# Optimization experiments

Hardware: AMD Instinct MI355X
Metric: run time of the kernel (lower is better)

## Reference

```python
import jax, jax.numpy as jnp
import numpy as np
import math

N, T, D, H = 64, 512, 1024, 1024

def setup_inputs() -> dict:
    key = jax.random.key(0)
    k1, k2, k3, k4 = jax.random.split(key, 4)
    x = jax.random.normal(k1, (N, T, D), dtype=jnp.float32)
    h0 = jax.random.normal(k2, (N, H), dtype=jnp.float32)
    Wx = jax.random.normal(k3, (D, 4 * H), dtype=jnp.float32) / math.sqrt(D)
    Wh = jax.random.normal(k4, (H, 4 * H), dtype=jnp.float32) / math.sqrt(H)
    b = jnp.zeros((4 * H,), dtype=jnp.float32)
    return {"x": x, "h0": h0, "Wx": Wx, "Wh": Wh, "b": b}

def lstm_forward(x, h0, Wx, Wh, b):
    Hd = h0.shape[1]
    # Precompute input-to-hidden contribution for all timesteps in one GEMM.
    xW = jnp.einsum('ntd,dg->ntg', x, Wx) + b  # (N, T, 4H)
    c0 = jnp.zeros_like(h0)

    def step(carry, xw_t):
        prev_h, prev_c = carry
        a = xw_t + prev_h @ Wh  # (N, 4H)
        i = jax.nn.sigmoid(a[:, :Hd])
        f = jax.nn.sigmoid(a[:, Hd:2 * Hd])
        o = jax.nn.sigmoid(a[:, 2 * Hd:3 * Hd])
        g = jnp.tanh(a[:, 3 * Hd:])
        next_c = f * prev_c + i * g
        next_h = o * jnp.tanh(next_c)
        return (next_h, next_c), next_h

    # scan over time axis: move T to leading dim
    (_, _), hs = jax.lax.scan(step, (h0, c0), jnp.swapaxes(xW, 0, 1))
    return jnp.swapaxes(hs, 0, 1)  # (N, T, H)

def reference(x, h0, Wx, Wh, b):
    return lstm_forward(x, h0, Wx, Wh, b)
```

## Files before the change

kernel.cpp:

```cpp
#include <hip/hip_runtime.h>


#define NB 64
#define TT 512
#define DD 1024
#define HH 1024
#define GG 4096
#define FSTRIDE 32
#define NCHUNK 256
#define CSTRIDE 8

using f32x4  = __attribute__((ext_vector_type(4))) float;
using bf16x8 = __attribute__((ext_vector_type(8))) __bf16;
using u16x4  = __attribute__((ext_vector_type(4))) unsigned short;

__device__ inline unsigned short f2bf(float x) {
  union { float f; unsigned u; } v; v.f = x;
  unsigned r = v.u + 0x7fffu + ((v.u >> 16) & 1u);
  return (unsigned short)(r >> 16);
}
__device__ inline float bfu2f(unsigned short u) {
  union { unsigned u; float f; } v; v.u = ((unsigned)u) << 16; return v.f;
}
__device__ inline float sigm(float x)     { return 1.0f / (1.0f + __expf(-x)); }
__device__ inline float tanhfast(float x) { return 1.0f - 2.0f / (__expf(2.0f * x) + 1.0f); }

__global__ __launch_bounds__(256) void tcast(const float* __restrict__ in,
                                             unsigned short* __restrict__ out,
                                             int rows, int cols) {
  __shared__ float tile[32][33];
  const int bx = blockIdx.x * 32;
  const int by = blockIdx.y * 32;
  const int tx = threadIdx.x;
  for (int i = threadIdx.y; i < 32; i += 8)
    tile[i][tx] = in[(size_t)(by + i) * cols + bx + tx];
  __syncthreads();
  for (int i = threadIdx.y; i < 32; i += 8)
    out[(size_t)(bx + i) * rows + by + tx] = f2bf(tile[tx][i]);
}

__global__ __launch_bounds__(256) void init_h(const float* __restrict__ h0,
                                              unsigned* __restrict__ hp0,
                                              unsigned* __restrict__ hp1,
                                              int* __restrict__ bar) {
  const int idx = blockIdx.x * 256 + threadIdx.x;
  const float v = h0[idx];
  const unsigned short hi = f2bf(v);
  const unsigned short lo = f2bf(v - bfu2f(hi));
  hp0[idx] = ((unsigned)hi << 16) | ((unsigned)(lo & 0xFFFEu));
  hp1[idx] = 1u;
  if (blockIdx.x == 0)
    for (int i = threadIdx.x; i < 256 * FSTRIDE + NCHUNK * CSTRIDE; i += 256)
      bar[i] = 0;
}

__global__ __launch_bounds__(512, 1) void lstm_fused(
    const float* __restrict__ x,
    const unsigned short* __restrict__ WxT,
    const unsigned short* __restrict__ WhT,
    const float* __restrict__ bvec,
    unsigned short* __restrict__ xw,
    unsigned* __restrict__ hp0, unsigned* __restrict__ hp1,
    float* __restrict__ out, int* __restrict__ bar) {
  __shared__ __align__(16) unsigned char smem[74240];
  const int tid = threadIdx.x;
  const int bid = blockIdx.x;
  int* cnt = bar + 256 * FSTRIDE;

  if (bid >= 128) {
    unsigned short (*As)[72] = (unsigned short(*)[72])smem;
    unsigned short (*Bs)[72] = (unsigned short(*)[72])(smem + 18432);
    const int gid  = bid - 128;
    const int wave = tid >> 6, lane = tid & 63;
    const int wm = (wave & 1) * 64, wn = (wave >> 1) * 32;
    const int lr = lane & 15, lk = (lane >> 4) * 8;

    for (int tau = gid; tau < NCHUNK * 32; tau += 128) {
      const int c  = tau >> 5;
      const int n  = tau & 31;
      const int m0 = c * 128;
      const int g0 = n * 128;
      f32x4 acc[4][2] = {};

      for (int kt = 0; kt < DD; kt += 64) {
#pragma unroll
        for (int it = 0; it < 4; ++it) {
          const int rl = it * 32 + (tid >> 4);
          const int c4 = (tid & 15) * 4;
          const int m  = m0 + rl;
          const size_t xrow = (size_t)(m & 63) * TT + (m >> 6);
          const float4 xv = *(const float4*)(x + xrow * DD + kt + c4);
          u16x4 us; us.x = f2bf(xv.x); us.y = f2bf(xv.y);
          us.z = f2bf(xv.z); us.w = f2bf(xv.w);
          *(u16x4*)&As[rl][c4] = us;
        }
#pragma unroll
        for (int it = 0; it < 2; ++it) {
          const int rl = it * 64 + (tid >> 3);
          const int c8 = (tid & 7) * 8;
          const uint4 wv = *(const uint4*)(WxT + (size_t)(g0 + rl) * DD + kt + c8);
          *(uint4*)&Bs[rl][c8] = wv;
        }
        __syncthreads();
#pragma unroll
        for (int ks = 0; ks < 2; ++ks) {
          const int kk = ks * 32 + lk;
          bf16x8 af[4], bfv[2];
#pragma unroll
          for (int mi = 0; mi < 4; ++mi) af[mi]  = *(const bf16x8*)&As[wm + mi * 16 + lr][kk];
#pragma unroll
          for (int ni = 0; ni < 2; ++ni) bfv[ni] = *(const bf16x8*)&Bs[wn + ni * 16 + lr][kk];
#pragma unroll
          for (int mi = 0; mi < 4; ++mi)
#pragma unroll
            for (int ni = 0; ni < 2; ++ni)
              acc[mi][ni] = __builtin_amdgcn_mfma_f32_16x16x32_bf16(af[mi], bfv[ni], acc[mi][ni], 0, 0, 0);
        }
        __syncthreads();
      }

#pragma unroll
      for (int mi = 0; mi < 4; ++mi) {
        const int row = m0 + wm + mi * 16 + ((lane >> 4) << 2);
#pragma unroll
        for (int ni = 0; ni < 2; ++ni) {
          const int col = g0 + wn + ni * 16 + lr;
          const float bb = bvec[col];
#pragma unroll
          for (int j = 0; j < 4; ++j)
            xw[(size_t)(row + j) * GG + col] = f2bf(acc[mi][ni][j] + bb);
        }
      }
      __syncthreads();
      if (tid == 0) {
        __builtin_amdgcn_fence(__ATOMIC_RELEASE, "agent");
        __hip_atomic_fetch_add(&cnt[c * CSTRIDE], 1,
                               __ATOMIC_RELAXED, __HIP_MEMORY_SCOPE_AGENT);
      }
    }
    return;
  }

  unsigned short (*As_hi)[1024] = (unsigned short(*)[1024])smem;
  unsigned short (*As_lo)[1024] = (unsigned short(*)[1024])(smem + 32768);
  float (*abuf)[16][34] = (float(*)[16][34])(smem + 65536);

  const int grp  = bid & 3;
  const int qid  = bid >> 2;
  const int r0   = grp * 16;
  const int j0   = qid * 32;
  const int w    = tid >> 6;
  const int gate = w & 3;
  const int ch   = w >> 2;
  const int lane = tid & 63;
  const int lr   = lane & 15;
  const int kslot = lane >> 4;
  const int sx   = lr & 7;
  const int srow = tid >> 5;
  const int swr  = srow & 7;
  const int re   = tid >> 5, ce = tid & 31;

  int* myflag = &bar[(grp * 32 + qid) * FSTRIDE];

  bf16x8 rB[32];
  {
    const unsigned short* wrow =
        WhT + ((size_t)(gate * HH + j0 + ch * 16 + lr)) * HH + kslot * 8;
#pragma unroll
    for (int ks = 0; ks < 32; ++ks)
      rB[ks] = *(const bf16x8*)&wrow[ks * 32];
  }

  float creg = 0.0f;

  const size_t xrowc = (size_t)(r0 + re) * GG + j0 + ce;
#define XWADDR(u, g) ((size_t)(u) * ((size_t)NB * GG) + xrowc + (size_t)(g) * HH)

  int last_c = 0;
  if (tid == 32) {
    while (__hip_atomic_load(&cnt[0], __ATOMIC_RELAXED, __HIP_MEMORY_SCOPE_AGENT) < 32)
      __builtin_amdgcn_s_sleep(2);
  }
  __syncthreads();
  unsigned short xc0 = xw[XWADDR(0, 0)];
  unsigned short xc1 = xw[XWADDR(0, 1)];
  unsigned short xc2 = xw[XWADDR(0, 2)];
  unsigned short xc3 = xw[XWADDR(0, 3)];

  for (int t = 0; t < TT; ++t) {
    unsigned* hp = (t & 1) ? hp1 : hp0;
    unsigned* np = (t & 1) ? hp0 : hp1;

    if (t > 0 && tid < 32) {
      const int* fp = &bar[(grp * 32 + tid) * FSTRIDE];
      int v = __hip_atomic_load(fp, __ATOMIC_RELAXED, __HIP_MEMORY_SCOPE_AGENT);
      while (v < t) {
        __builtin_amdgcn_s_sleep(2);
        v = __hip_atomic_load(fp, __ATOMIC_RELAXED, __HIP_MEMORY_SCOPE_AGENT);
      }
    }
    if (tid == 32) {
      const int u = (t + 1 < TT) ? (t + 1) : (TT - 1);
      const int cn = u >> 1;
      if (cn > last_c) {
        while (__hip_atomic_load(&cnt[cn * CSTRIDE],
                                 __ATOMIC_RELAXED, __HIP_MEMORY_SCOPE_AGENT) < 32)
          __builtin_amdgcn_s_sleep(2);
        last_c = cn;
      }
    }
    __syncthreads();

    const unsigned* hrow = hp + (size_t)(r0 + srow) * HH;
    const int c0 = 0 * 32 + (tid & 31), c1 = 1 * 32 + (tid & 31);
    const int c2 = 2 * 32 + (tid & 31), c3 = 3 * 32 + (tid & 31);
    const unsigned* p0 = hrow + c0 * 8;
    const unsigned* p1 = hrow + c1 * 8;
    const unsigned* p2 = hrow + c2 * 8;
    const unsigned* p3 = hrow + c3 * 8;
    const unsigned expect = (unsigned)((t >> 1) & 1);
    uint4 q0, q1, q2, q3, q4, q5, q6, q7;
    for (;;) {
      asm volatile(
          "global_load_dwordx4 %0, %[a0], off sc0 sc1\n\t"
          "global_load_dwordx4 %1, %[a0], off offset:16 sc0 sc1\n\t"
          "global_load_dwordx4 %2, %[a1], off sc0 sc1\n\t"
          "global_load_dwordx4 %3, %[a1], off offset:16 sc0 sc1\n\t"
          "global_load_dwordx4 %4, %[a2], off sc0 sc1\n\t"
          "global_load_dwordx4 %5, %[a2], off offset:16 sc0 sc1\n\t"
          "global_load_dwordx4 %6, %[a3], off sc0 sc1\n\t"
          "global_load_dwordx4 %7, %[a3], off offset:16 sc0 sc1\n\t"
          "s_waitcnt vmcnt(0)"
          : "=&v"(q0), "=&v"(q1), "=&v"(q2), "=&v"(q3),
            "=&v"(q4), "=&v"(q5), "=&v"(q6), "=&v"(q7)
          : [a0] "v"(p0), [a1] "v"(p1), [a2] "v"(p2), [a3] "v"(p3)
          : "memory");
      const unsigned av = q0.x & q0.y & q0.z & q0.w & q1.x & q1.y & q1.z & q1.w &
                          q2.x & q2.y & q2.z & q2.w & q3.x & q3.y & q3.z & q3.w &
                          q4.x & q4.y & q4.z & q4.w & q5.x & q5.y & q5.z & q5.w &
                          q6.x & q6.y & q6.z & q6.w & q7.x & q7.y & q7.z & q7.w;
      const unsigned ov = q0.x | q0.y | q0.z | q0.w | q1.x | q1.y | q1.z | q1.w |
                          q2.x | q2.y | q2.z | q2.w | q3.x | q3.y | q3.z | q3.w |
                          q4.x | q4.y | q4.z | q4.w | q5.x | q5.y | q5.z | q5.w |
                          q6.x | q6.y | q6.z | q6.w | q7.x | q7.y | q7.z | q7.w;
      const unsigned chk = expect ? av : ~ov;
      if (chk & 1u) break;
      __builtin_amdgcn_s_sleep(1);
    }

#define UNPACK(QA, QB, CC)                                                    \
    {                                                                         \
      const int sc = (CC) ^ swr;                                              \
      uint4 HI, LO;                                                           \
      HI.x = (QA.x >> 16) | (QA.y & 0xffff0000u);                             \
      HI.y = (QA.z >> 16) | (QA.w & 0xffff0000u);                             \
      HI.z = (QB.x >> 16) | (QB.y & 0xffff0000u);                             \
      HI.w = (QB.z >> 16) | (QB.w & 0xffff0000u);                             \
      LO.x = (QA.x & 0xffffu) | (QA.y << 16);                                 \
      LO.y = (QA.z & 0xffffu) | (QA.w << 16);                                 \
      LO.z = (QB.x & 0xffffu) | (QB.y << 16);                                 \
      LO.w = (QB.z & 0xffffu) | (QB.w << 16);                                 \
      *(uint4*)&As_hi[srow][sc * 8] = HI;                                     \
      *(uint4*)&As_lo[srow][sc * 8] = LO;                                     \
    }
    UNPACK(q0, q1, c0) UNPACK(q2, q3, c1) UNPACK(q4, q5, c2) UNPACK(q6, q7, c3)
#undef UNPACK
    __syncthreads();

    const int tn = (t + 1 < TT) ? t + 1 : t;
    const unsigned short nx0 = xw[XWADDR(tn, 0)];
    const unsigned short nx1 = xw[XWADDR(tn, 1)];
    const unsigned short nx2 = xw[XWADDR(tn, 2)];
    const unsigned short nx3 = xw[XWADDR(tn, 3)];

    f32x4 aHE = {}, aHO = {}, aLE = {}, aLO = {};
#pragma unroll
    for (int ks = 0; ks < 32; ks += 2) {
      const int cc0 = ((ks)     * 4 + kslot) ^ sx;
      const int cc1 = ((ks + 1) * 4 + kslot) ^ sx;
      const bf16x8 ah0 = *(const bf16x8*)&As_hi[lr][cc0 * 8];
      const bf16x8 al0 = *(const bf16x8*)&As_lo[lr][cc0 * 8];
      const bf16x8 ah1 = *(const bf16x8*)&As_hi[lr][cc1 * 8];
      const bf16x8 al1 = *(const bf16x8*)&As_lo[lr][cc1 * 8];
      aHE = __builtin_amdgcn_mfma_f32_16x16x32_bf16(ah0, rB[ks],     aHE, 0, 0, 0);
      aLE = __builtin_amdgcn_mfma_f32_16x16x32_bf16(al0, rB[ks],     aLE, 0, 0, 0);
      aHO = __builtin_amdgcn_mfma_f32_16x16x32_bf16(ah1, rB[ks + 1], aHO, 0, 0, 0);
      aLO = __builtin_amdgcn_mfma_f32_16x16x32_bf16(al1, rB[ks + 1], aLO, 0, 0, 0);
    }
    const f32x4 accv = (aHE + aHO) + (aLE + aLO);

#pragma unroll
    for (int j = 0; j < 4; ++j)
      abuf[gate][(lane >> 4) * 4 + j][ch * 16 + lr] = accv[j];
    __syncthreads();

    const float ai = abuf[0][re][ce] + bfu2f(xc0);
    const float af = abuf[1][re][ce] + bfu2f(xc1);
    const float ao = abuf[2][re][ce] + bfu2f(xc2);
    const float ag = abuf[3][re][ce] + bfu2f(xc3);

    const float gi = sigm(ai), gf = sigm(af), go = sigm(ao), gg = tanhfast(ag);
    creg = gf * creg + gi * gg;
    const float hn = go * tanhfast(creg);

    out[((size_t)(r0 + re) * TT + t) * HH + j0 + ce] = hn;
    const unsigned short hi = f2bf(hn);
    const unsigned short lo = f2bf(hn - bfu2f(hi));
    const unsigned tag = (unsigned)(((t + 1) >> 1) & 1);
    const unsigned pack = ((unsigned)hi << 16) | ((unsigned)(lo & 0xFFFEu) | tag);
    __hip_atomic_store(&np[(size_t)(r0 + re) * HH + j0 + ce], pack,
                       __ATOMIC_RELAXED, __HIP_MEMORY_SCOPE_AGENT);

    xc0 = nx0; xc1 = nx1; xc2 = nx2; xc3 = nx3;

    if (t + 1 < TT) {
      __syncthreads();
      if (tid == 0)
        __hip_atomic_store(myflag, t + 1, __ATOMIC_RELAXED, __HIP_MEMORY_SCOPE_AGENT);
    }
  }
#undef XWADDR
}

extern "C" void kernel_launch(void* const* d_in, const int* in_sizes, int n_in,
                              void* d_out, int out_size, void* d_ws, size_t ws_size,
                              hipStream_t stream) {
  const float* x  = (const float*)d_in[0];
  const float* h0 = (const float*)d_in[1];
  const float* Wx = (const float*)d_in[2];
  const float* Wh = (const float*)d_in[3];
  const float* b  = (const float*)d_in[4];
  float* out = (float*)d_out;

  const size_t xw_elems = (size_t)NB * TT * GG;
  const size_t wT_elems = (size_t)GG * DD;
  const size_t NH       = (size_t)NB * HH;

  unsigned short* xw  = (unsigned short*)d_ws;
  unsigned short* WxT = xw + xw_elems;
  unsigned short* WhT = WxT + wT_elems;
  unsigned* hp0 = (unsigned*)(WhT + wT_elems);
  unsigned* hp1 = hp0 + NH;
  int* bar = (int*)(hp1 + NH);

  tcast<<<dim3(GG / 32, DD / 32), dim3(32, 8), 0, stream>>>(Wx, WxT, DD, GG);
  tcast<<<dim3(GG / 32, HH / 32), dim3(32, 8), 0, stream>>>(Wh, WhT, HH, GG);
  init_h<<<NB * HH / 256, 256, 0, stream>>>(h0, hp0, hp1, bar);

  lstm_fused<<<256, 512, 0, stream>>>(x, WxT, WhT, b, xw, hp0, hp1, out, bar);
}
```

Before: 2.681 ms.

## Fuse weight transpose-cast into persistent LSTM kernel and busy-spin step flags

Removes the two separate transpose-and-cast kernel launches. The 128 GEMM blocks inside the fused kernel now transpose Wx and Wh to bf16 themselves and publish completion through a new device-wide counter. Recurrent blocks wait on that counter before loading Wh into registers. The per-step flag polling also drops s_sleep and spins tightly, aiming to cut wake-up latency per timestep at the cost of more memory traffic from polling.

```diff
diff --git a/kernel.cpp b/kernel.cpp
--- a/kernel.cpp
+++ b/kernel.cpp
@@ -24,20 +24,6 @@
 }
 __device__ inline float sigm(float x)     { return 1.0f / (1.0f + __expf(-x)); }
 __device__ inline float tanhfast(float x) { return 1.0f - 2.0f / (__expf(2.0f * x) + 1.0f); }
-
-__global__ __launch_bounds__(256) void tcast(const float* __restrict__ in,
-                                             unsigned short* __restrict__ out,
-                                             int rows, int cols) {
-  __shared__ float tile[32][33];
-  const int bx = blockIdx.x * 32;
-  const int by = blockIdx.y * 32;
-  const int tx = threadIdx.x;
-  for (int i = threadIdx.y; i < 32; i += 8)
-    tile[i][tx] = in[(size_t)(by + i) * cols + bx + tx];
-  __syncthreads();
-  for (int i = threadIdx.y; i < 32; i += 8)
-    out[(size_t)(bx + i) * rows + by + tx] = f2bf(tile[tx][i]);
-}
 
 __global__ __launch_bounds__(256) void init_h(const float* __restrict__ h0,
                                               unsigned* __restrict__ hp0,
@@ -50,27 +36,67 @@
   hp0[idx] = ((unsigned)hi << 16) | ((unsigned)(lo & 0xFFFEu));
   hp1[idx] = 1u;
   if (blockIdx.x == 0)
-    for (int i = threadIdx.x; i < 256 * FSTRIDE + NCHUNK * CSTRIDE; i += 256)
+    for (int i = threadIdx.x; i < 256 * FSTRIDE + NCHUNK * CSTRIDE + 8; i += 256)
       bar[i] = 0;
 }
 
 __global__ __launch_bounds__(512, 1) void lstm_fused(
     const float* __restrict__ x,
-    const unsigned short* __restrict__ WxT,
-    const unsigned short* __restrict__ WhT,
+    const float* __restrict__ Wx,
+    const float* __restrict__ Wh,
     const float* __restrict__ bvec,
+    unsigned short* __restrict__ WxT,
+    unsigned short* __restrict__ WhT,
     unsigned short* __restrict__ xw,
     unsigned* __restrict__ hp0, unsigned* __restrict__ hp1,
     float* __restrict__ out, int* __restrict__ bar) {
   __shared__ __align__(16) unsigned char smem[74240];
   const int tid = threadIdx.x;
   const int bid = blockIdx.x;
-  int* cnt = bar + 256 * FSTRIDE;
+  int* cnt   = bar + 256 * FSTRIDE;
+  int* wTcnt = cnt + NCHUNK * CSTRIDE;
 
   if (bid >= 128) {
+    const int gid = bid - 128;
+
+    {
+      const int g0t = gid * 32;
+      const int gq  = (tid & 7) * 4;
+      const int kb  = (tid >> 3) * 16;
+#define TRANSP(SRC, DST)                                                      \
+      {                                                                       \
+        unsigned short col[4][16];                                            \
+        _Pragma("unroll")                                                     \
+        for (int i = 0; i < 16; ++i) {                                        \
+          const float4 f4 = *(const float4*)(SRC + (size_t)(kb + i) * GG + g0t + gq); \
+          col[0][i] = f2bf(f4.x); col[1][i] = f2bf(f4.y);                     \
+          col[2][i] = f2bf(f4.z); col[3][i] = f2bf(f4.w);                     \
+        }                                                                     \
+        _Pragma("unroll")                                                     \
+        for (int j = 0; j < 4; ++j) {                                         \
+          *(u16x4*)(DST + (size_t)(g0t + gq + j) * DD + kb)      = *(u16x4*)&col[j][0];  \
+          *(u16x4*)(DST + (size_t)(g0t + gq + j) * DD + kb + 4)  = *(u16x4*)&col[j][4];  \
+          *(u16x4*)(DST + (size_t)(g0t + gq + j) * DD + kb + 8)  = *(u16x4*)&col[j][8];  \
+          *(u16x4*)(DST + (size_t)(g0t + gq + j) * DD + kb + 12) = *(u16x4*)&col[j][12]; \
+        }                                                                     \
+      }
+      TRANSP(Wx, WxT)
+      TRANSP(Wh, WhT)
+#undef TRANSP
+    }
+    __syncthreads();
+    if (tid == 0) {
+      __builtin_amdgcn_fence(__ATOMIC_RELEASE, "agent");
+      __hip_atomic_fetch_add(wTcnt, 1, __ATOMIC_RELAXED, __HIP_MEMORY_SCOPE_AGENT);
+    }
+    if (tid == 0) {
+      while (__hip_atomic_load(wTcnt, __ATOMIC_RELAXED, __HIP_MEMORY_SCOPE_AGENT) < 128)
+        __builtin_amdgcn_s_sleep(2);
+    }
+    __syncthreads();
+
     unsigned short (*As)[72] = (unsigned short(*)[72])smem;
     unsigned short (*Bs)[72] = (unsigned short(*)[72])(smem + 18432);
-    const int gid  = bid - 128;
     const int wave = tid >> 6, lane = tid & 63;
     const int wm = (wave & 1) * 64, wn = (wave >> 1) * 32;
     const int lr = lane & 15, lk = (lane >> 4) * 8;
@@ -162,6 +188,12 @@
 
   int* myflag = &bar[(grp * 32 + qid) * FSTRIDE];
 
+  if (tid == 0) {
+    while (__hip_atomic_load(wTcnt, __ATOMIC_RELAXED, __HIP_MEMORY_SCOPE_AGENT) < 128)
+      __builtin_amdgcn_s_sleep(2);
+  }
+  __syncthreads();
+
   bf16x8 rB[32];
   {
     const unsigned short* wrow =
@@ -193,11 +225,7 @@
 
     if (t > 0 && tid < 32) {
       const int* fp = &bar[(grp * 32 + tid) * FSTRIDE];
-      int v = __hip_atomic_load(fp, __ATOMIC_RELAXED, __HIP_MEMORY_SCOPE_AGENT);
-      while (v < t) {
-        __builtin_amdgcn_s_sleep(2);
-        v = __hip_atomic_load(fp, __ATOMIC_RELAXED, __HIP_MEMORY_SCOPE_AGENT);
-      }
+      while (__hip_atomic_load(fp, __ATOMIC_RELAXED, __HIP_MEMORY_SCOPE_AGENT) < t) {}
     }
     if (tid == 32) {
       const int u = (t + 1 < TT) ? (t + 1) : (TT - 1);
@@ -343,9 +371,7 @@
   unsigned* hp1 = hp0 + NH;
   int* bar = (int*)(hp1 + NH);
 
-  tcast<<<dim3(GG / 32, DD / 32), dim3(32, 8), 0, stream>>>(Wx, WxT, DD, GG);
-  tcast<<<dim3(GG / 32, HH / 32), dim3(32, 8), 0, stream>>>(Wh, WhT, HH, GG);
   init_h<<<NB * HH / 256, 256, 0, stream>>>(h0, hp0, hp1, bar);
-
-  lstm_fused<<<256, 512, 0, stream>>>(x, WxT, WhT, b, xw, hp0, hp1, out, bar);
-}
+  lstm_fused<<<256, 512, 0, stream>>>(x, Wx, Wh, b, WxT, WhT, xw,
+                                      hp0, hp1, out, bar);
+}
```

Result: no change. 2.676 ms (-0.2%).
